# Performance work log

Measured on AMD Instinct MI355X. Metric: run time of the kernel, lower is better.

The kernel has to match this reference:

```python
import jax, jax.numpy as jnp
import numpy as np

N = 50000
E = 800000
IN_CH = 128
HID = 64
HEADS = 4
OUT_CH = 64
NEG_SLOPE = 0.2


def add_self_loops(edge_index, num_nodes):
    loops = jnp.arange(num_nodes, dtype=edge_index.dtype)
    src = jnp.concatenate([edge_index[0], loops])
    dst = jnp.concatenate([edge_index[1], loops])
    return src, dst


def gat_layer(x, src, dst, W, a_src, a_dst, b, heads, out_ch, concat):
    n = x.shape[0]
    h = (x @ W).reshape(n, heads, out_ch)              # [N,H,C]
    al_src = jnp.einsum('nhc,hc->nh', h, a_src)        # [N,H]
    al_dst = jnp.einsum('nhc,hc->nh', h, a_dst)        # [N,H]
    e = jax.nn.leaky_relu(al_src[src] + al_dst[dst], NEG_SLOPE)  # [Et,H]
    # segment softmax over incoming edges of each destination node
    m = jax.ops.segment_max(e, dst, num_segments=n)
    ex = jnp.exp(e - m[dst])
    denom = jax.ops.segment_sum(ex, dst, num_segments=n)
    alpha = ex / (denom[dst] + 1e-16)                  # [Et,H]
    msg = h[src] * alpha[:, :, None]                   # [Et,H,C]
    out = jax.ops.segment_sum(msg, dst, num_segments=n)  # [N,H,C]
    if concat:
        out = out.reshape(n, heads * out_ch)
    else:
        out = out.mean(axis=1)
    return out + b


def setup_inputs() -> dict:
    key = jax.random.key(0)
    ks = jax.random.split(key, 10)
    x = jax.random.normal(ks[0], (N, IN_CH), dtype=jnp.float32)
    edge_index = jax.random.randint(ks[1], (2, E), 0, N, dtype=jnp.int64)
    s1 = 1.0 / np.sqrt(IN_CH)
    W1 = jax.random.normal(ks[2], (IN_CH, HEADS * HID), dtype=jnp.float32) * s1
    a_src1 = jax.random.normal(ks[3], (HEADS, HID), dtype=jnp.float32) * 0.1
    a_dst1 = jax.random.normal(ks[4], (HEADS, HID), dtype=jnp.float32) * 0.1
    b1 = jnp.zeros((HEADS * HID,), dtype=jnp.float32)
    s2 = 1.0 / np.sqrt(HEADS * HID)
    W2 = jax.random.normal(ks[5], (HEADS * HID, OUT_CH), dtype=jnp.float32) * s2
    a_src2 = jax.random.normal(ks[6], (1, OUT_CH), dtype=jnp.float32) * 0.1
    a_dst2 = jax.random.normal(ks[7], (1, OUT_CH), dtype=jnp.float32) * 0.1
    b2 = jnp.zeros((OUT_CH,), dtype=jnp.float32)
    return {"x": x, "edge_index": edge_index, "W1": W1, "a_src1": a_src1,
            "a_dst1": a_dst1, "b1": b1, "W2": W2, "a_src2": a_src2,
            "a_dst2": a_dst2, "b2": b2}


def reference(x, edge_index, W1, a_src1, a_dst1, b1, W2, a_src2, a_dst2, b2):
    src, dst = add_self_loops(edge_index, x.shape[0])
    h = gat_layer(x, src, dst, W1, a_src1, a_dst1, b1, HEADS, HID, True)
    h = jax.nn.elu(h)
    h = gat_layer(h, src, dst, W2, a_src2, a_dst2, b2, 1, OUT_CH, False)
    return jax.nn.elu(h)
```

## Files before the change

kernel.cpp:

```cpp
#include <hip/hip_runtime.h>
#include <hip/hip_bf16.h>
#include <cstdint>
#include <cstddef>


typedef float f32x4 __attribute__((ext_vector_type(4)));
typedef __fp16 f16x8 __attribute__((ext_vector_type(8)));

static __device__ __forceinline__ float lrelu02(float x) { return x > 0.f ? x : 0.2f * x; }
static __device__ __forceinline__ float eluf(float x)    { return x > 0.f ? x : __expf(x) - 1.f; }

static __device__ __forceinline__ int block_flag(const int* __restrict__ ei, int e,
                                                 int* sflag) {
    int t = threadIdx.x;
    if (t < 64) {
        int m = e < 64 ? e : 64;
        int z = (t < m && ei[2 * t + 1] == 0) ? 1 : 0;
        unsigned long long bal = __ballot(z);
        if (t == 0) *sflag = (__popcll(bal) >= m / 2 + 1) ? 1 : 0;
    }
    __syncthreads();
    return *sflag;
}

__global__ __launch_bounds__(256) void k1_kernel(const float* __restrict__ A,
                                                 const float* __restrict__ W1,
                                                 __fp16* __restrict__ C,
                                                 const float* __restrict__ a_src,
                                                 const float* __restrict__ a_dst,
                                                 float* __restrict__ als,
                                                 float* __restrict__ ald,
                                                 const int* __restrict__ ei,
                                                 int* __restrict__ deg,
                                                 const float* __restrict__ W2,
                                                 __fp16* __restrict__ w2t,
                                                 int M, int e, int gb, int hb) {
    __shared__ __fp16 sm[17920];
    int b = blockIdx.x;
    int t = threadIdx.x;
    if (b >= gb) {
        if (b < gb + hb) {
            int f = block_flag(ei, e, (int*)sm);
            int i = (b - gb) * 256 + t;
            if (i < e) {
                int d = f ? ei[2 * (e + i)] : ei[e + i];
                atomicAdd(&deg[d], 1);
            }
        } else {
            int j = (b - gb - hb) * 256 + t;
            if (j < 16384) {
                int nn = j >> 8, k = j & 255;
                w2t[j] = (__fp16)W2[k * 64 + nn];
            }
        }
        return;
    }
    #define AS(r, c)  sm[(r) * 40 + (c)]
    #define BST(r, c) sm[2560 + (r) * 40 + (c)]
    #define CS(r, c)  sm[(r) * 264 + (c)]
    float* sa = (float*)(sm + 16896);
    float* sd = (float*)(sm + 17408);
    int wv = t >> 6, l = t & 63;
    int lm = l & 15, kq = l >> 4;
    int bm = b * 64;
    sa[t] = a_src[t];
    sd[t] = a_dst[t];
    f32x4 zero = {0.f, 0.f, 0.f, 0.f};
    f32x4 acc[4][4] = {{zero, zero, zero, zero}, {zero, zero, zero, zero},
                       {zero, zero, zero, zero}, {zero, zero, zero, zero}};
    int arow = t >> 2, achunk = (t & 3) * 8;
    for (int k0 = 0; k0 < 128; k0 += 32) {
        {
            int gr = bm + arow;
            f16x8 av;
            if (gr < M) {
                const float* ap = A + (size_t)gr * 128 + k0 + achunk;
                float4 a0 = *(const float4*)(ap + 0);
                float4 a1 = *(const float4*)(ap + 4);
                av[0] = (__fp16)a0.x; av[1] = (__fp16)a0.y; av[2] = (__fp16)a0.z; av[3] = (__fp16)a0.w;
                av[4] = (__fp16)a1.x; av[5] = (__fp16)a1.y; av[6] = (__fp16)a1.z; av[7] = (__fp16)a1.w;
            } else { f16x8 z = {0,0,0,0,0,0,0,0}; av = z; }
            *(f16x8*)&AS(arow, achunk) = av;
        }
        {
            #pragma unroll
            for (int bc = 0; bc < 4; ++bc) {
                f16x8 bh;
                #pragma unroll
                for (int j = 0; j < 8; ++j)
                    bh[j] = (__fp16)W1[(size_t)(k0 + bc * 8 + j) * 256 + t];
                *(f16x8*)&BST(t, bc * 8) = bh;
            }
        }
        __syncthreads();
        #pragma unroll
        for (int nt = 0; nt < 4; ++nt) {
            f16x8 bfrag = *(const f16x8*)&BST(wv * 64 + nt * 16 + lm, kq * 8);
            #pragma unroll
            for (int mt = 0; mt < 4; ++mt) {
                f16x8 afrag = *(const f16x8*)&AS(mt * 16 + lm, kq * 8);
                acc[mt][nt] = __builtin_amdgcn_mfma_f32_16x16x32_f16(afrag, bfrag, acc[mt][nt], 0, 0, 0);
            }
        }
        __syncthreads();
    }
    #pragma unroll
    for (int mt = 0; mt < 4; ++mt)
        #pragma unroll
        for (int nt = 0; nt < 4; ++nt)
            #pragma unroll
            for (int r = 0; r < 4; ++r)
                CS(mt * 16 + kq * 4 + r, wv * 64 + nt * 16 + lm) = (__fp16)acc[mt][nt][r];
    __syncthreads();
    {
        int row = t >> 2, head = t & 3;
        int gr = bm + row;
        f16x8 c[8];
        #pragma unroll
        for (int q = 0; q < 8; ++q) c[q] = *(const f16x8*)&CS(row, head * 64 + q * 8);
        float ps = 0.f, pd = 0.f;
        #pragma unroll
        for (int q = 0; q < 8; ++q)
            #pragma unroll
            for (int j = 0; j < 8; ++j) {
                float v = (float)c[q][j];
                ps += v * sa[head * 64 + q * 8 + j];
                pd += v * sd[head * 64 + q * 8 + j];
            }
        if (gr < M) {
            f16x8* gp = (f16x8*)(C + (size_t)gr * 256 + head * 64);
            #pragma unroll
            for (int q = 0; q < 8; ++q) gp[q] = c[q];
            als[gr * 4 + head] = ps;
            ald[gr * 4 + head] = pd;
        }
    }
    #undef AS
    #undef BST
    #undef CS
}

__global__ __launch_bounds__(256) void scan_blocks_kernel(const int* __restrict__ deg,
                                                          int* __restrict__ loc,
                                                          int* __restrict__ bsum, int n) {
    __shared__ int wsum[4];
    int t = threadIdx.x, lane = t & 63, w = t >> 6;
    int base = blockIdx.x * 1024 + t * 4;
    int4 v = make_int4(0, 0, 0, 0);
    if (base + 3 < n) {
        v = *(const int4*)(deg + base);
        v.x += 1; v.y += 1; v.z += 1; v.w += 1;
    } else {
        if (base < n) v.x = deg[base] + 1;
        if (base + 1 < n) v.y = deg[base + 1] + 1;
        if (base + 2 < n) v.z = deg[base + 2] + 1;
        if (base + 3 < n) v.w = deg[base + 3] + 1;
    }
    int s = v.x + v.y + v.z + v.w;
    int incl = s;
    #pragma unroll
    for (int d = 1; d < 64; d <<= 1) { int o = __shfl_up(incl, d); if (lane >= d) incl += o; }
    if (lane == 63) wsum[w] = incl;
    __syncthreads();
    int woff = 0;
    for (int k = 0; k < w; ++k) woff += wsum[k];
    int excl = woff + incl - s;
    if (base < n) {
        int e0 = excl, e1 = e0 + v.x, e2 = e1 + v.y, e3 = e2 + v.z;
        loc[base] = e0;
        if (base + 1 < n) loc[base + 1] = e1;
        if (base + 2 < n) loc[base + 2] = e2;
        if (base + 3 < n) loc[base + 3] = e3;
    }
    if (t == 255) bsum[blockIdx.x] = woff + incl;
}

__global__ void scan_add_kernel(int* __restrict__ rowptr, const int* __restrict__ bsum,
                                int* __restrict__ cursor, int n, int nb) {
    int i = blockIdx.x * 256 + threadIdx.x;
    if (i < n) {
        int chunk = i >> 10;
        int off = 0;
        for (int k = 0; k < chunk; ++k) off += bsum[k];
        int v = rowptr[i] + off;
        rowptr[i] = v;
        cursor[i] = v;
    } else if (i == n) {
        int tot = 0;
        for (int k = 0; k < nb; ++k) tot += bsum[k];
        rowptr[n] = tot;
    }
}

__global__ __launch_bounds__(256) void scatter_kernel(const int* __restrict__ ei,
                                                      int* __restrict__ cursor,
                                                      int* __restrict__ sidx,
                                                      int e, int et) {
    __shared__ int sflag;
    int f = block_flag(ei, e, &sflag);
    int i = blockIdx.x * 256 + threadIdx.x;
    if (i >= et) return;
    int s, d;
    if (i < e) {
        s = f ? ei[2 * i] : ei[i];
        d = f ? ei[2 * (e + i)] : ei[e + i];
    } else { s = d = i - e; }
    int pos = atomicAdd(&cursor[d], 1);
    sidx[pos] = s;
}

__global__ __launch_bounds__(256) void agg1_kernel(const __fp16* __restrict__ h1,
                                                   const int* __restrict__ sidx,
                                                   const int* __restrict__ rowptr,
                                                   const float* __restrict__ als,
                                                   const float* __restrict__ ald,
                                                   const float* __restrict__ b1,
                                                   __fp16* __restrict__ x2, int n) {
    int t = threadIdx.x, wv = t >> 6, l = t & 63;
    int node = blockIdx.x * 4 + wv;
    if (node >= n) return;
    int le = l & 31, halfE = l >> 5;
    int head = le >> 3;
    float aldn = ald[node * 4 + head];
    int p0 = rowptr[node], p1 = rowptr[node + 1];
    float acc[8] = {0.f, 0.f, 0.f, 0.f, 0.f, 0.f, 0.f, 0.f};
    float accw = 0.f;
    auto body = [&](int p) {
        int s = sidx[p];
        float wt = __expf(lrelu02(als[s * 4 + head] + aldn));
        accw += wt;
        f16x8 r = *(const f16x8*)(h1 + (size_t)s * 256 + le * 8);
        #pragma unroll
        for (int j = 0; j < 8; ++j) acc[j] += wt * (float)r[j];
    };
    int p = p0 + halfE;
    for (; p + 6 < p1; p += 8) { body(p); body(p + 2); body(p + 4); body(p + 6); }
    for (; p < p1; p += 2) body(p);
    #pragma unroll
    for (int j = 0; j < 8; ++j) acc[j] += __shfl_down(acc[j], 32);
    accw += __shfl_down(accw, 32);
    if (l < 32) {
        float rd = 1.f / (accw + 1e-16f);
        f16x8 o;
        #pragma unroll
        for (int j = 0; j < 8; ++j) {
            float v = acc[j] * rd + b1[le * 8 + j];
            o[j] = (__fp16)eluf(v);
        }
        *(f16x8*)(x2 + (size_t)node * 256 + le * 8) = o;
    }
}

__global__ __launch_bounds__(256) void gemm2_kernel(const __fp16* __restrict__ A,
                                                    const __fp16* __restrict__ w2t,
                                                    __fp16* __restrict__ C,
                                                    const float* __restrict__ a_src,
                                                    const float* __restrict__ a_dst,
                                                    float* __restrict__ als,
                                                    float* __restrict__ ald, int M) {
    __shared__ __fp16 sm[9216];
    #define AS(r, c)  sm[(r) * 72 + (c)]
    #define BST(r, c) sm[4608 + (r) * 72 + (c)]
    #define CS(r, c)  sm[(r) * 72 + (c)]
    int t = threadIdx.x;
    int wv = t >> 6, l = t & 63;
    int lm = l & 15, kq = l >> 4;
    int bm = blockIdx.x * 64;
    f32x4 zero = {0.f, 0.f, 0.f, 0.f};
    f32x4 acc[4] = {zero, zero, zero, zero};
    int arow = t >> 2, akp = (t & 3) * 16;
    int bn = t & 63, bkc = (t >> 6) * 16;
    for (int k0 = 0; k0 < 256; k0 += 64) {
        {
            int gr = bm + arow;
            f16x8 av0, av1;
            if (gr < M) {
                const __fp16* ap = A + (size_t)gr * 256 + k0 + akp;
                av0 = *(const f16x8*)(ap);
                av1 = *(const f16x8*)(ap + 8);
            } else { f16x8 z = {0,0,0,0,0,0,0,0}; av0 = z; av1 = z; }
            *(f16x8*)&AS(arow, akp) = av0;
            *(f16x8*)&AS(arow, akp + 8) = av1;
        }
        {
            const __fp16* bp = w2t + (size_t)bn * 256 + k0 + bkc;
            *(f16x8*)&BST(bn, bkc) = *(const f16x8*)(bp);
            *(f16x8*)&BST(bn, bkc + 8) = *(const f16x8*)(bp + 8);
        }
        __syncthreads();
        #pragma unroll
        for (int ki = 0; ki < 2; ++ki) {
            int kc = ki * 32 + kq * 8;
            f16x8 bfrag = *(const f16x8*)&BST(wv * 16 + lm, kc);
            #pragma unroll
            for (int mt = 0; mt < 4; ++mt) {
                f16x8 afrag = *(const f16x8*)&AS(mt * 16 + lm, kc);
                acc[mt] = __builtin_amdgcn_mfma_f32_16x16x32_f16(afrag, bfrag, acc[mt], 0, 0, 0);
            }
        }
        __syncthreads();
    }
    #pragma unroll
    for (int mt = 0; mt < 4; ++mt)
        #pragma unroll
        for (int r = 0; r < 4; ++r)
            CS(mt * 16 + kq * 4 + r, wv * 16 + lm) = (__fp16)acc[mt][r];
    __syncthreads();
    {
        int row = t >> 2, ch = (t & 3) * 16;
        int gr = bm + row;
        f16x8 c0 = *(const f16x8*)&CS(row, ch);
        f16x8 c1 = *(const f16x8*)&CS(row, ch + 8);
        if (gr < M) {
            f16x8* gp = (f16x8*)(C + (size_t)gr * 64 + ch);
            gp[0] = c0; gp[1] = c1;
        }
        float ps = 0.f, pd = 0.f;
        #pragma unroll
        for (int j = 0; j < 8; ++j) {
            float v0 = (float)c0[j], v1 = (float)c1[j];
            ps += v0 * a_src[ch + j] + v1 * a_src[ch + 8 + j];
            pd += v0 * a_dst[ch + j] + v1 * a_dst[ch + 8 + j];
        }
        ps += __shfl_down(ps, 2); ps += __shfl_down(ps, 1);
        pd += __shfl_down(pd, 2); pd += __shfl_down(pd, 1);
        if ((t & 3) == 0 && gr < M) {
            als[gr] = ps;
            ald[gr] = pd;
        }
    }
    #undef AS
    #undef BST
    #undef CS
}

__global__ __launch_bounds__(256) void agg2_kernel(const __fp16* __restrict__ h2,
                                                   const int* __restrict__ sidx,
                                                   const int* __restrict__ rowptr,
                                                   const float* __restrict__ als,
                                                   const float* __restrict__ ald,
                                                   const float* __restrict__ b2,
                                                   float* __restrict__ out, int n) {
    int t = threadIdx.x, wv = t >> 6, l = t & 63;
    int node = blockIdx.x * 4 + wv;
    if (node >= n) return;
    int slot = l >> 3, cq = l & 7;
    float aldn = ald[node];
    int p0 = rowptr[node], p1 = rowptr[node + 1];
    float acc[8] = {0.f, 0.f, 0.f, 0.f, 0.f, 0.f, 0.f, 0.f};
    float accw = 0.f;
    auto body = [&](int p) {
        int s = sidx[p];
        float wt = __expf(lrelu02(als[s] + aldn));
        accw += wt;
        f16x8 r = *(const f16x8*)(h2 + (size_t)s * 64 + cq * 8);
        #pragma unroll
        for (int j = 0; j < 8; ++j) acc[j] += wt * (float)r[j];
    };
    int p = p0 + slot;
    for (; p + 24 < p1; p += 32) { body(p); body(p + 8); body(p + 16); body(p + 24); }
    for (; p < p1; p += 8) body(p);
    #pragma unroll
    for (int j = 0; j < 8; ++j) {
        acc[j] += __shfl_down(acc[j], 32);
        acc[j] += __shfl_down(acc[j], 16);
        acc[j] += __shfl_down(acc[j], 8);
    }
    accw += __shfl_down(accw, 32);
    accw += __shfl_down(accw, 16);
    accw += __shfl_down(accw, 8);
    if (l < 8) {
        float rd = 1.f / (accw + 1e-16f);
        float4 o0, o1;
        o0.x = eluf(acc[0] * rd + b2[cq * 8 + 0]);
        o0.y = eluf(acc[1] * rd + b2[cq * 8 + 1]);
        o0.z = eluf(acc[2] * rd + b2[cq * 8 + 2]);
        o0.w = eluf(acc[3] * rd + b2[cq * 8 + 3]);
        o1.x = eluf(acc[4] * rd + b2[cq * 8 + 4]);
        o1.y = eluf(acc[5] * rd + b2[cq * 8 + 5]);
        o1.z = eluf(acc[6] * rd + b2[cq * 8 + 6]);
        o1.w = eluf(acc[7] * rd + b2[cq * 8 + 7]);
        float4* gp = (float4*)(out + (size_t)node * 64 + cq * 8);
        gp[0] = o0; gp[1] = o1;
    }
}

extern "C" void kernel_launch(void* const* d_in, const int* in_sizes, int n_in,
                              void* d_out, int out_size, void* d_ws, size_t ws_size,
                              hipStream_t stream) {
    const float* x   = (const float*)d_in[0];
    const int*   ei  = (const int*)d_in[1];
    const float* W1  = (const float*)d_in[2];
    const float* as1 = (const float*)d_in[3];
    const float* ad1 = (const float*)d_in[4];
    const float* b1  = (const float*)d_in[5];
    const float* W2  = (const float*)d_in[6];
    const float* as2 = (const float*)d_in[7];
    const float* ad2 = (const float*)d_in[8];
    const float* b2  = (const float*)d_in[9];
    float* out = (float*)d_out;

    const int n  = in_sizes[0] / 128;
    const int e  = in_sizes[1] / 2;
    const int et = e + n;

    char* w = (char*)d_ws;
    size_t off = 0;
    auto take = [&](size_t bytes) -> void* {
        void* p = w + off;
        off = (off + bytes + 255) & ~(size_t)255;
        return p;
    };
    __fp16* h1h = (__fp16*)take((size_t)n * 256 * 2);
    __fp16* x2h = (__fp16*)take((size_t)n * 256 * 2);
    __fp16* h2h = (__fp16*)take((size_t)n * 64 * 2);
    __fp16* w2t = (__fp16*)take((size_t)64 * 256 * 2);
    float* al1s = (float*)take((size_t)n * 4 * 4);
    float* al1d = (float*)take((size_t)n * 4 * 4);
    float* al2s = (float*)take((size_t)n * 4);
    float* al2d = (float*)take((size_t)n * 4);
    int* deg    = (int*)take((size_t)(n + 1) * 4);
    int* rowptr = (int*)take((size_t)(n + 1) * 4);
    int* cursor = (int*)take((size_t)(n + 1) * 4);
    int* sidx   = (int*)take((size_t)et * 4);
    int* bsum   = (int*)take(256);

    const int gb = (n + 63) / 64;
    const int hb = (e + 255) / 256;
    const int pb = (16384 + 255) / 256;
    const int nb = (n + 1023) / 1024;

    hipMemsetAsync(deg, 0, (size_t)(n + 1) * 4, stream);
    k1_kernel<<<gb + hb + pb, 256, 0, stream>>>(x, W1, h1h, as1, ad1, al1s, al1d,
                                                ei, deg, W2, w2t, n, e, gb, hb);
    scan_blocks_kernel<<<nb, 256, 0, stream>>>(deg, rowptr, bsum, n);
    scan_add_kernel<<<(n + 1 + 255) / 256, 256, 0, stream>>>(rowptr, bsum, cursor, n, nb);
    scatter_kernel<<<(et + 255) / 256, 256, 0, stream>>>(ei, cursor, sidx, e, et);
    agg1_kernel<<<(n + 3) / 4, 256, 0, stream>>>(h1h, sidx, rowptr, al1s, al1d, b1, x2h, n);
    gemm2_kernel<<<(n + 63) / 64, 256, 0, stream>>>(x2h, w2t, h2h, as2, ad2, al2s, al2d, n);
    agg2_kernel<<<(n + 3) / 4, 256, 0, stream>>>(h2h, sidx, rowptr, al2s, al2d, b2, out, n);
}
```

Baseline: 290.3 us.

## Record atomic order in degree pass, drop cursor atomics, fuse scatter with GEMM1

The degree-counting pass now saves each edge's atomicAdd return value as its slot within the destination row. This lets the CSR scatter place edges with no second round of atomics. The scan-add and scatter steps are merged into the layer-1 GEMM launch, cutting two kernel launches and letting the graph work overlap with the matmul. W1 is pre-transposed to fp16 in the first kernel, and the GEMM now uses a 64-wide K tile with contiguous B loads. The cost is an extra ord buffer of E ints and a larger shared-memory footprint in the fused kernel, which may lower occupancy.

```diff
diff --git a/kernel.cpp b/kernel.cpp
--- a/kernel.cpp
+++ b/kernel.cpp
@@ -10,138 +10,45 @@
 static __device__ __forceinline__ float lrelu02(float x) { return x > 0.f ? x : 0.2f * x; }
 static __device__ __forceinline__ float eluf(float x)    { return x > 0.f ? x : __expf(x) - 1.f; }
 
-static __device__ __forceinline__ int block_flag(const int* __restrict__ ei, int e,
-                                                 int* sflag) {
-    int t = threadIdx.x;
-    if (t < 64) {
-        int m = e < 64 ? e : 64;
-        int z = (t < m && ei[2 * t + 1] == 0) ? 1 : 0;
-        unsigned long long bal = __ballot(z);
-        if (t == 0) *sflag = (__popcll(bal) >= m / 2 + 1) ? 1 : 0;
-    }
-    __syncthreads();
-    return *sflag;
-}
-
-__global__ __launch_bounds__(256) void k1_kernel(const float* __restrict__ A,
+__global__ __launch_bounds__(256) void kA_kernel(const int* __restrict__ ei,
+                                                 int* __restrict__ deg,
+                                                 int* __restrict__ ord,
                                                  const float* __restrict__ W1,
-                                                 __fp16* __restrict__ C,
-                                                 const float* __restrict__ a_src,
-                                                 const float* __restrict__ a_dst,
-                                                 float* __restrict__ als,
-                                                 float* __restrict__ ald,
-                                                 const int* __restrict__ ei,
-                                                 int* __restrict__ deg,
                                                  const float* __restrict__ W2,
+                                                 __fp16* __restrict__ w1t,
                                                  __fp16* __restrict__ w2t,
-                                                 int M, int e, int gb, int hb) {
-    __shared__ __fp16 sm[17920];
-    int b = blockIdx.x;
-    int t = threadIdx.x;
-    if (b >= gb) {
-        if (b < gb + hb) {
-            int f = block_flag(ei, e, (int*)sm);
-            int i = (b - gb) * 256 + t;
-            if (i < e) {
-                int d = f ? ei[2 * (e + i)] : ei[e + i];
-                atomicAdd(&deg[d], 1);
-            }
-        } else {
-            int j = (b - gb - hb) * 256 + t;
-            if (j < 16384) {
-                int nn = j >> 8, k = j & 255;
-                w2t[j] = (__fp16)W2[k * 64 + nn];
-            }
-        }
-        return;
-    }
-    #define AS(r, c)  sm[(r) * 40 + (c)]
-    #define BST(r, c) sm[2560 + (r) * 40 + (c)]
-    #define CS(r, c)  sm[(r) * 264 + (c)]
-    float* sa = (float*)(sm + 16896);
-    float* sd = (float*)(sm + 17408);
-    int wv = t >> 6, l = t & 63;
-    int lm = l & 15, kq = l >> 4;
-    int bm = b * 64;
-    sa[t] = a_src[t];
-    sd[t] = a_dst[t];
-    f32x4 zero = {0.f, 0.f, 0.f, 0.f};
-    f32x4 acc[4][4] = {{zero, zero, zero, zero}, {zero, zero, zero, zero},
-                       {zero, zero, zero, zero}, {zero, zero, zero, zero}};
-    int arow = t >> 2, achunk = (t & 3) * 8;
-    for (int k0 = 0; k0 < 128; k0 += 32) {
-        {
-            int gr = bm + arow;
-            f16x8 av;
-            if (gr < M) {
-                const float* ap = A + (size_t)gr * 128 + k0 + achunk;
-                float4 a0 = *(const float4*)(ap + 0);
-                float4 a1 = *(const float4*)(ap + 4);
-                av[0] = (__fp16)a0.x; av[1] = (__fp16)a0.y; av[2] = (__fp16)a0.z; av[3] = (__fp16)a0.w;
-                av[4] = (__fp16)a1.x; av[5] = (__fp16)a1.y; av[6] = (__fp16)a1.z; av[7] = (__fp16)a1.w;
-            } else { f16x8 z = {0,0,0,0,0,0,0,0}; av = z; }
-            *(f16x8*)&AS(arow, achunk) = av;
-        }
-        {
-            #pragma unroll
-            for (int bc = 0; bc < 4; ++bc) {
-                f16x8 bh;
-                #pragma unroll
-                for (int j = 0; j < 8; ++j)
-                    bh[j] = (__fp16)W1[(size_t)(k0 + bc * 8 + j) * 256 + t];
-                *(f16x8*)&BST(t, bc * 8) = bh;
-            }
+                                                 int e, int hb) {
+    __shared__ int sflag;
+    int b = blockIdx.x, t = threadIdx.x;
+    if (b < hb) {
+        if (t < 64) {
+            int m = e < 64 ? e : 64;
+            int z = (t < m && ei[2 * t + 1] == 0) ? 1 : 0;
+            unsigned long long bal = __ballot(z);
+            if (t == 0) sflag = (__popcll(bal) >= m / 2 + 1) ? 1 : 0;
         }
         __syncthreads();
-        #pragma unroll
-        for (int nt = 0; nt < 4; ++nt) {
-            f16x8 bfrag = *(const f16x8*)&BST(wv * 64 + nt * 16 + lm, kq * 8);
-            #pragma unroll
-            for (int mt = 0; mt < 4; ++mt) {
-                f16x8 afrag = *(const f16x8*)&AS(mt * 16 + lm, kq * 8);
-                acc[mt][nt] = __builtin_amdgcn_mfma_f32_16x16x32_f16(afrag, bfrag, acc[mt][nt], 0, 0, 0);
-            }
-        }
-        __syncthreads();
-    }
-    #pragma unroll
-    for (int mt = 0; mt < 4; ++mt)
-        #pragma unroll
-        for (int nt = 0; nt < 4; ++nt)
-            #pragma unroll
-            for (int r = 0; r < 4; ++r)
-                CS(mt * 16 + kq * 4 + r, wv * 64 + nt * 16 + lm) = (__fp16)acc[mt][nt][r];
-    __syncthreads();
-    {
-        int row = t >> 2, head = t & 3;
-        int gr = bm + row;
-        f16x8 c[8];
-        #pragma unroll
-        for (int q = 0; q < 8; ++q) c[q] = *(const f16x8*)&CS(row, head * 64 + q * 8);
-        float ps = 0.f, pd = 0.f;
-        #pragma unroll
-        for (int q = 0; q < 8; ++q)
-            #pragma unroll
-            for (int j = 0; j < 8; ++j) {
-                float v = (float)c[q][j];
-                ps += v * sa[head * 64 + q * 8 + j];
-                pd += v * sd[head * 64 + q * 8 + j];
-            }
-        if (gr < M) {
-            f16x8* gp = (f16x8*)(C + (size_t)gr * 256 + head * 64);
-            #pragma unroll
-            for (int q = 0; q < 8; ++q) gp[q] = c[q];
-            als[gr * 4 + head] = ps;
-            ald[gr * 4 + head] = pd;
-        }
-    }
-    #undef AS
-    #undef BST
-    #undef CS
+        int f = sflag;
+        int i = b * 256 + t;
+        if (i < e) {
+            int d = f ? ei[2 * (e + i)] : ei[e + i];
+            ord[i] = atomicAdd(&deg[d], 1);
+        }
+    } else {
+        int j = (b - hb) * 256 + t;
+        if (j < 32768) {
+            int nn = j >> 7, k = j & 127;
+            w1t[j] = (__fp16)W1[k * 256 + nn];
+        } else if (j < 49152) {
+            int jj = j - 32768;
+            int nn = jj >> 8, k = jj & 255;
+            w2t[jj] = (__fp16)W2[k * 64 + nn];
+        }
+    }
 }
 
 __global__ __launch_bounds__(256) void scan_blocks_kernel(const int* __restrict__ deg,
-                                                          int* __restrict__ loc,
+                                                          int* __restrict__ rloc,
                                                           int* __restrict__ bsum, int n) {
     __shared__ int wsum[4];
     int t = threadIdx.x, lane = t & 63, w = t >> 6;
@@ -167,46 +74,171 @@
     int excl = woff + incl - s;
     if (base < n) {
         int e0 = excl, e1 = e0 + v.x, e2 = e1 + v.y, e3 = e2 + v.z;
-        loc[base] = e0;
-        if (base + 1 < n) loc[base + 1] = e1;
-        if (base + 2 < n) loc[base + 2] = e2;
-        if (base + 3 < n) loc[base + 3] = e3;
+        rloc[base] = e0;
+        if (base + 1 < n) rloc[base + 1] = e1;
+        if (base + 2 < n) rloc[base + 2] = e2;
+        if (base + 3 < n) rloc[base + 3] = e3;
     }
     if (t == 255) bsum[blockIdx.x] = woff + incl;
 }
 
-__global__ void scan_add_kernel(int* __restrict__ rowptr, const int* __restrict__ bsum,
-                                int* __restrict__ cursor, int n, int nb) {
-    int i = blockIdx.x * 256 + threadIdx.x;
-    if (i < n) {
-        int chunk = i >> 10;
-        int off = 0;
-        for (int k = 0; k < chunk; ++k) off += bsum[k];
-        int v = rowptr[i] + off;
-        rowptr[i] = v;
-        cursor[i] = v;
-    } else if (i == n) {
-        int tot = 0;
-        for (int k = 0; k < nb; ++k) tot += bsum[k];
-        rowptr[n] = tot;
-    }
-}
-
-__global__ __launch_bounds__(256) void scatter_kernel(const int* __restrict__ ei,
-                                                      int* __restrict__ cursor,
-                                                      int* __restrict__ sidx,
-                                                      int e, int et) {
-    __shared__ int sflag;
-    int f = block_flag(ei, e, &sflag);
-    int i = blockIdx.x * 256 + threadIdx.x;
-    if (i >= et) return;
-    int s, d;
-    if (i < e) {
-        s = f ? ei[2 * i] : ei[i];
-        d = f ? ei[2 * (e + i)] : ei[e + i];
-    } else { s = d = i - e; }
-    int pos = atomicAdd(&cursor[d], 1);
-    sidx[pos] = s;
+__global__ __launch_bounds__(256) void kB_kernel(const float* __restrict__ A,
+                                                 const __fp16* __restrict__ w1t,
+                                                 __fp16* __restrict__ C,
+                                                 const float* __restrict__ a_src,
+                                                 const float* __restrict__ a_dst,
+                                                 float* __restrict__ als,
+                                                 float* __restrict__ ald,
+                                                 const int* __restrict__ ei,
+                                                 const int* __restrict__ rloc,
+                                                 const int* __restrict__ bsum,
+                                                 const int* __restrict__ deg,
+                                                 const int* __restrict__ ord,
+                                                 int* __restrict__ rowptr,
+                                                 int* __restrict__ sidx,
+                                                 int M, int e, int et, int n, int nb,
+                                                 int gb, int sb) {
+    __shared__ __fp16 sm[24064];
+    int b = blockIdx.x, t = threadIdx.x;
+    if (b >= gb) {
+        if (b < gb + sb) {
+            int i = (b - gb) * 256 + t;
+            if (i < n) {
+                int chunk = i >> 10;
+                int off = 0;
+                for (int k = 0; k < chunk; ++k) off += bsum[k];
+                rowptr[i] = rloc[i] + off;
+            } else if (i == n) {
+                int tot = 0;
+                for (int k = 0; k < nb; ++k) tot += bsum[k];
+                rowptr[n] = tot;
+            }
+        } else {
+            int* sflag = (int*)sm;
+            int* pref  = (int*)sm + 16;
+            if (t < 64) {
+                int m = e < 64 ? e : 64;
+                int z = (t < m && ei[2 * t + 1] == 0) ? 1 : 0;
+                unsigned long long bal = __ballot(z);
+                if (t == 0) *sflag = (__popcll(bal) >= m / 2 + 1) ? 1 : 0;
+                int v = (t < nb) ? bsum[t] : 0;
+                int incl = v;
+                #pragma unroll
+                for (int dd = 1; dd < 64; dd <<= 1) {
+                    int o = __shfl_up(incl, dd);
+                    if (t >= dd) incl += o;
+                }
+                pref[t] = incl - v;
+            }
+            __syncthreads();
+            int f = *sflag;
+            int i = (b - gb - sb) * 256 + t;
+            if (i < et) {
+                int s, d, loc;
+                if (i < e) {
+                    s = f ? ei[2 * i] : ei[i];
+                    d = f ? ei[2 * (e + i)] : ei[e + i];
+                    loc = ord[i];
+                } else {
+                    d = s = i - e;
+                    loc = deg[d];
+                }
+                sidx[rloc[d] + pref[d >> 10] + loc] = s;
+            }
+        }
+        return;
+    }
+    #define AS(r, c)  sm[(r) * 72 + (c)]
+    #define BST(r, c) sm[4608 + (r) * 72 + (c)]
+    #define CS(r, c)  sm[(r) * 264 + (c)]
+    float* sa = (float*)(sm + 23040);
+    float* sd = (float*)(sm + 23552);
+    int wv = t >> 6, l = t & 63;
+    int lm = l & 15, kq = l >> 4;
+    int bm = b * 64;
+    sa[t] = a_src[t];
+    sd[t] = a_dst[t];
+    f32x4 zero = {0.f, 0.f, 0.f, 0.f};
+    f32x4 acc[4][4] = {{zero, zero, zero, zero}, {zero, zero, zero, zero},
+                       {zero, zero, zero, zero}, {zero, zero, zero, zero}};
+    int arow = t >> 2, akp = (t & 3) * 16;
+    for (int k0 = 0; k0 < 128; k0 += 64) {
+        {
+            int gr = bm + arow;
+            f16x8 av0, av1;
+            if (gr < M) {
+                const float* ap = A + (size_t)gr * 128 + k0 + akp;
+                float4 a0 = *(const float4*)(ap + 0);
+                float4 a1 = *(const float4*)(ap + 4);
+                float4 a2 = *(const float4*)(ap + 8);
+                float4 a3 = *(const float4*)(ap + 12);
+                av0[0] = (__fp16)a0.x; av0[1] = (__fp16)a0.y; av0[2] = (__fp16)a0.z; av0[3] = (__fp16)a0.w;
+                av0[4] = (__fp16)a1.x; av0[5] = (__fp16)a1.y; av0[6] = (__fp16)a1.z; av0[7] = (__fp16)a1.w;
+                av1[0] = (__fp16)a2.x; av1[1] = (__fp16)a2.y; av1[2] = (__fp16)a2.z; av1[3] = (__fp16)a2.w;
+                av1[4] = (__fp16)a3.x; av1[5] = (__fp16)a3.y; av1[6] = (__fp16)a3.z; av1[7] = (__fp16)a3.w;
+            } else {
+                f16x8 z = {0,0,0,0,0,0,0,0}; av0 = z; av1 = z;
+            }
+            *(f16x8*)&AS(arow, akp) = av0;
+            *(f16x8*)&AS(arow, akp + 8) = av1;
+        }
+        {
+            const __fp16* bp = w1t + (size_t)t * 128 + k0;
+            #pragma unroll
+            for (int c = 0; c < 8; ++c)
+                *(f16x8*)&BST(t, c * 8) = *(const f16x8*)(bp + c * 8);
+        }
+        __syncthreads();
+        #pragma unroll
+        for (int ki = 0; ki < 2; ++ki) {
+            int kc = ki * 32 + kq * 8;
+            f16x8 af[4];
+            #pragma unroll
+            for (int mt = 0; mt < 4; ++mt) af[mt] = *(const f16x8*)&AS(mt * 16 + lm, kc);
+            #pragma unroll
+            for (int nt = 0; nt < 4; ++nt) {
+                f16x8 bfrag = *(const f16x8*)&BST(wv * 64 + nt * 16 + lm, kc);
+                #pragma unroll
+                for (int mt = 0; mt < 4; ++mt)
+                    acc[mt][nt] = __builtin_amdgcn_mfma_f32_16x16x32_f16(af[mt], bfrag, acc[mt][nt], 0, 0, 0);
+            }
+        }
+        __syncthreads();
+    }
+    #pragma unroll
+    for (int mt = 0; mt < 4; ++mt)
+        #pragma unroll
+        for (int nt = 0; nt < 4; ++nt)
+            #pragma unroll
+            for (int r = 0; r < 4; ++r)
+                CS(mt * 16 + kq * 4 + r, wv * 64 + nt * 16 + lm) = (__fp16)acc[mt][nt][r];
+    __syncthreads();
+    {
+        int row = t >> 2, head = t & 3;
+        int gr = bm + row;
+        f16x8 c[8];
+        #pragma unroll
+        for (int q = 0; q < 8; ++q) c[q] = *(const f16x8*)&CS(row, head * 64 + q * 8);
+        float ps = 0.f, pd = 0.f;
+        #pragma unroll
+        for (int q = 0; q < 8; ++q)
+            #pragma unroll
+            for (int j = 0; j < 8; ++j) {
+                float v = (float)c[q][j];
+                ps += v * sa[head * 64 + q * 8 + j];
+                pd += v * sd[head * 64 + q * 8 + j];
+            }
+        if (gr < M) {
+            f16x8* gp = (f16x8*)(C + (size_t)gr * 256 + head * 64);
+            #pragma unroll
+            for (int q = 0; q < 8; ++q) gp[q] = c[q];
+            als[gr * 4 + head] = ps;
+            ald[gr * 4 + head] = pd;
+        }
+    }
+    #undef AS
+    #undef BST
+    #undef CS
 }
 
 __global__ __launch_bounds__(256) void agg1_kernel(const __fp16* __restrict__ h1,
@@ -414,28 +446,32 @@
     __fp16* h1h = (__fp16*)take((size_t)n * 256 * 2);
     __fp16* x2h = (__fp16*)take((size_t)n * 256 * 2);
     __fp16* h2h = (__fp16*)take((size_t)n * 64 * 2);
+    __fp16* w1t = (__fp16*)take((size_t)256 * 128 * 2);
     __fp16* w2t = (__fp16*)take((size_t)64 * 256 * 2);
     float* al1s = (float*)take((size_t)n * 4 * 4);
     float* al1d = (float*)take((size_t)n * 4 * 4);
     float* al2s = (float*)take((size_t)n * 4);
     float* al2d = (float*)take((size_t)n * 4);
     int* deg    = (int*)take((size_t)(n + 1) * 4);
+    int* rloc   = (int*)take((size_t)(n + 1) * 4);
     int* rowptr = (int*)take((size_t)(n + 1) * 4);
-    int* cursor = (int*)take((size_t)(n + 1) * 4);
+    int* ord    = (int*)take((size_t)e * 4);
     int* sidx   = (int*)take((size_t)et * 4);
     int* bsum   = (int*)take(256);
 
+    const int hb = (e + 255) / 256;
+    const int pb = (49152 + 255) / 256;
+    const int nb = (n + 1023) / 1024;
     const int gb = (n + 63) / 64;
-    const int hb = (e + 255) / 256;
-    const int pb = (16384 + 255) / 256;
-    const int nb = (n + 1023) / 1024;
+    const int sb = (n + 1 + 255) / 256;
+    const int cb = (et + 255) / 256;
 
     hipMemsetAsync(deg, 0, (size_t)(n + 1) * 4, stream);
-    k1_kernel<<<gb + hb + pb, 256, 0, stream>>>(x, W1, h1h, as1, ad1, al1s, al1d,
-                                                ei, deg, W2, w2t, n, e, gb, hb);
-    scan_blocks_kernel<<<nb, 256, 0, stream>>>(deg, rowptr, bsum, n);
-    scan_add_kernel<<<(n + 1 + 255) / 256, 256, 0, stream>>>(rowptr, bsum, cursor, n, nb);
-    scatter_kernel<<<(et + 255) / 256, 256, 0, stream>>>(ei, cursor, sidx, e, et);
+    kA_kernel<<<hb + pb, 256, 0, stream>>>(ei, deg, ord, W1, W2, w1t, w2t, e, hb);
+    scan_blocks_kernel<<<nb, 256, 0, stream>>>(deg, rloc, bsum, n);
+    kB_kernel<<<gb + sb + cb, 256, 0, stream>>>(x, w1t, h1h, as1, ad1, al1s, al1d,
+                                                ei, rloc, bsum, deg, ord, rowptr, sidx,
+                                                n, e, et, n, nb, gb, sb);
     agg1_kernel<<<(n + 3) / 4, 256, 0, stream>>>(h1h, sidx, rowptr, al1s, al1d, b1, x2h, n);
     gemm2_kernel<<<(n + 63) / 64, 256, 0, stream>>>(x2h, w2t, h2h, as2, ad2, al2s, al2d, n);
     agg2_kernel<<<(n + 3) / 4, 256, 0, stream>>>(h2h, sidx, rowptr, al2s, al2d, b2, out, n);
```

After: 257.7 us, median of 2. 11.2% less time.
